# Performance work log

Hardware: AMD Instinct MI355X
Metric: run time of the kernel (lower is better)

Reference implementation:

```python
import jax, jax.numpy as jnp
import numpy as np

B, N, FIN, FOUT, E = 2, 50000, 128, 64, 800000


def setup_inputs() -> dict:
    key = jax.random.key(0)
    ks = jax.random.split(key, 7)
    x = jax.random.normal(ks[0], (B, N, FIN), dtype=jnp.float32)
    W = jax.random.normal(ks[1], (FIN, FOUT), dtype=jnp.float32) * (1.0 / np.sqrt(FIN))
    W_self = jax.random.normal(ks[2], (FIN, FOUT), dtype=jnp.float32) * (1.0 / np.sqrt(FIN))
    b_self = jax.random.normal(ks[3], (FOUT,), dtype=jnp.float32) * 0.01
    edge_row = jax.random.randint(ks[4], (E,), 0, N, dtype=jnp.int32)
    edge_col = jax.random.randint(ks[5], (E,), 0, N, dtype=jnp.int32)
    edge_val = jax.random.uniform(ks[6], (E,), dtype=jnp.float32)
    return {"x": x, "W": W, "W_self": W_self, "b_self": b_self,
            "edge_row": edge_row, "edge_col": edge_col, "edge_val": edge_val}


def reference(x, W, W_self, b_self, edge_row, edge_col, edge_val):
    # x: (B, N, FIN); adjacency in COO form: out[r] += val * in[c]
    Bn, Nn, _ = x.shape
    Fo = W.shape[1]
    x_trans = jnp.einsum("bnf,fo->bno", x, W)               # (B, N, FOUT), no bias
    # Same layout trick as torch: sparse.mm over (N, B*FOUT)
    xr = x_trans.transpose(1, 0, 2).reshape(Nn, Bn * Fo)    # (N, B*FOUT)
    msgs = edge_val[:, None] * xr[edge_col]                  # (E, B*FOUT) gather
    agg = jax.ops.segment_sum(msgs, edge_row, num_segments=Nn)  # (N, B*FOUT) scatter-add
    agg = agg.reshape(Nn, Bn, Fo).transpose(1, 0, 2)         # (B, N, FOUT)
    self_c = jnp.einsum("bnf,fo->bno", x, W_self) + b_self   # Linear with bias
    return jax.nn.relu(self_c + agg)
```

## Files before the change

### kernel.cpp

```cpp
#include <hip/hip_runtime.h>
#include <hip/hip_fp16.h>

#define Bc   2
#define Nn   50000
#define FINc 128
#define FOUTc 64
#define Mtot (Bc * Nn)
#define CCOMB 128
#define GB 1563
#define CAP 64

#define NRNG   128
#define NBUCK  391
#define ABLK   256
#define ATHR   1024
#define RECCAP 3200

typedef __bf16 bf16x8 __attribute__((ext_vector_type(8)));
typedef float  f32x4  __attribute__((ext_vector_type(4)));

static __device__ inline unsigned short f2bf(float f) {
    unsigned int u = __float_as_uint(f);
    u += 0x7fffu + ((u >> 16) & 1u);
    return (unsigned short)(u >> 16);
}

__global__ __launch_bounds__(256) void prep(
    const float* __restrict__ W, const float* __restrict__ Ws,
    unsigned short* __restrict__ Bp)
{
    const int idx = blockIdx.x * 256 + threadIdx.x;
    const int lane = idx & 63;
    const int kt   = (idx >> 6) & 3;
    const int nt   = idx >> 8;
    const int n    = nt * 16 + (lane & 15);
    const int k0   = kt * 32 + (lane >> 4) * 8;
    unsigned short o8[8];
#pragma unroll
    for (int j = 0; j < 8; ++j) {
        const int f = k0 + j;
        const float v = (n < 64) ? W[f * FOUTc + n] : Ws[f * FOUTc + (n - 64)];
        o8[j] = f2bf(v);
    }
    *(uint4*)&Bp[(size_t)idx * 8] = *(uint4*)o8;
}

__global__ __launch_bounds__(256) void gemm(
    const float* __restrict__ x, const unsigned short* __restrict__ Bp,
    const float* __restrict__ bself,
    unsigned short* __restrict__ xrb, float* __restrict__ outp)
{
    const int gb   = blockIdx.x;
    const int lane = threadIdx.x & 63;
    const int quad = lane >> 4;
    const int mbase = gb * 64 + (threadIdx.x >> 6) * 16;

    const int mrow   = mbase + (lane & 15);
    const int mclamp = (mrow < Mtot) ? mrow : (Mtot - 1);
    const float* __restrict__ xrow = &x[(size_t)mclamp * FINc + quad * 8];

    float4 xv[8];
#pragma unroll
    for (int kt = 0; kt < 4; ++kt) {
        xv[2 * kt]     = *(const float4*)&xrow[kt * 32];
        xv[2 * kt + 1] = *(const float4*)&xrow[kt * 32 + 4];
    }

    f32x4 acc[8] = {};

#pragma unroll
    for (int kt = 0; kt < 4; ++kt) {
        const float4 xa = xv[2 * kt];
        const float4 xb = xv[2 * kt + 1];
        bf16x8 bf;
        bf[0] = (__bf16)xa.x; bf[1] = (__bf16)xa.y;
        bf[2] = (__bf16)xa.z; bf[3] = (__bf16)xa.w;
        bf[4] = (__bf16)xb.x; bf[5] = (__bf16)xb.y;
        bf[6] = (__bf16)xb.z; bf[7] = (__bf16)xb.w;

        const bf16x8* __restrict__ abase =
            (const bf16x8*)&Bp[(size_t)(kt * 64 + lane) * 8];
#pragma unroll
        for (int nt = 0; nt < 8; ++nt) {
            const bf16x8 af = abase[nt * 4 * 64];
            acc[nt] = __builtin_amdgcn_mfma_f32_16x16x32_bf16(af, bf, acc[nt], 0, 0, 0);
        }
    }

    const int m = mbase + (lane & 15);
    if (m < Mtot) {
        const int bb = (m >= Nn) ? 1 : 0;
        const int n = m - bb * Nn;
        unsigned short* __restrict__ xp = &xrb[(size_t)n * CCOMB + bb * FOUTc];
        const int cq = quad * 4;
#pragma unroll
        for (int nt = 0; nt < 4; ++nt) {
            const int c = nt * 16 + cq;
            unsigned short h[4];
            h[0] = f2bf(acc[nt][0]); h[1] = f2bf(acc[nt][1]);
            h[2] = f2bf(acc[nt][2]); h[3] = f2bf(acc[nt][3]);
            *(uint2*)&xp[c] = *(uint2*)h;
        }
        float* __restrict__ op = &outp[(size_t)m * FOUTc];
#pragma unroll
        for (int nt = 4; nt < 8; ++nt) {
            const int o = (nt - 4) * 16 + cq;
            const float4 b4 = *(const float4*)&bself[o];
            float4 v;
            v.x = acc[nt][0] + b4.x; v.y = acc[nt][1] + b4.y;
            v.z = acc[nt][2] + b4.z; v.w = acc[nt][3] + b4.w;
            *(float4*)&op[o] = v;
        }
    }
}

__global__ __launch_bounds__(1024) void bin_a(
    const int* __restrict__ erow, const int* __restrict__ ecol,
    const float* __restrict__ evalv, unsigned int* __restrict__ cntm,
    unsigned int* __restrict__ ofsm, uint2* __restrict__ stage,
    int E, int ec)
{
    __shared__ unsigned int hist[512];
    __shared__ unsigned int incl[512];
    __shared__ unsigned int cur[NBUCK];
    __shared__ unsigned int recs[RECCAP * 2];

    const int tid = threadIdx.x;
    const int ord = blockIdx.x;
    const int e0 = ord * ec;
    int e1 = e0 + ec; if (e1 > E) e1 = E;
    if (e1 - e0 > RECCAP) e1 = e0 + RECCAP;
    const int tot = e1 - e0;

    if (tid < 512) hist[tid] = 0u;
    __syncthreads();

    for (int e = e0 + tid; e < e1; e += ATHR)
        atomicAdd(&hist[erow[e] >> 7], 1u);
    __syncthreads();

    if (tid < 512) incl[tid] = hist[tid];
    __syncthreads();
    for (int off = 1; off < 512; off <<= 1) {
        const unsigned int a0 = (tid < 512 && tid >= off) ? incl[tid - off] : 0u;
        __syncthreads();
        if (tid < 512) incl[tid] += a0;
        __syncthreads();
    }

    for (int i = tid; i < NBUCK; i += ATHR) {
        const unsigned int c = hist[i];
        const unsigned int x0 = incl[i] - c;
        cur[i] = x0;
        cntm[(size_t)ord * NBUCK + i] = c;
        ofsm[(size_t)ord * NBUCK + i] = x0;
    }
    __syncthreads();

    for (int e = e0 + tid; e < e1; e += ATHR) {
        const int   r = erow[e];
        const int   c = ecol[e];
        const float v = evalv[e];
        const int  nb = r >> 7;
        const unsigned int k = atomicAdd(&cur[nb], 1u);
        recs[2 * k]     = ((unsigned int)__half_as_ushort(__float2half(v)) << 17) |
                          (unsigned int)c;
        recs[2 * k + 1] = (unsigned int)(r & 127);
    }
    __syncthreads();

    uint2* __restrict__ chunk = &stage[(size_t)ord * RECCAP];
    for (int j = tid; j < tot; j += ATHR)
        chunk[j] = make_uint2(recs[2 * j], recs[2 * j + 1]);
}

__global__ __launch_bounds__(256) void bin_b(
    const unsigned int* __restrict__ cntm, const unsigned int* __restrict__ ofsm,
    const uint2* __restrict__ stage,
    unsigned int* __restrict__ cvp, int* __restrict__ cntp)
{
    __shared__ unsigned int lists[NRNG * CAP];
    __shared__ unsigned int lcnt[NRNG];

    const int tid = threadIdx.x;
    const int nb  = blockIdx.x;
    const int row0 = nb << 7;
    int nrows = Nn - row0; if (nrows > NRNG) nrows = NRNG;

    for (int i = tid; i < NRNG; i += 256) lcnt[i] = 0u;
    __syncthreads();

    {
        const unsigned int c = cntm[(size_t)tid * NBUCK + nb];
        const unsigned int o = ofsm[(size_t)tid * NBUCK + nb];
        const uint2* __restrict__ run = &stage[(size_t)tid * RECCAP + o];
        for (unsigned int j = 0; j < c; ++j) {
            const uint2 rec = run[j];
            const int rl = (int)(rec.y & 127u);
            const unsigned int k = atomicAdd(&lcnt[rl], 1u);
            if (k < CAP) lists[(rl << 6) + k] = rec.x;
        }
    }
    __syncthreads();

    unsigned int* __restrict__ dst = &cvp[(size_t)row0 << 6];
    const int words = nrows << 6;
    for (int i = tid; i < words; i += 256) dst[i] = lists[i];
    for (int rl = tid; rl < nrows; rl += 256) {
        const unsigned int c = lcnt[rl];
        cntp[(size_t)(row0 + rl) * 16] = (int)(c < CAP ? c : CAP);
    }
}

#define GATHP(W, PRED, ACC)                                                   \
    {                                                                         \
        const unsigned int w = (W);                                           \
        unsigned int col = w & 0x1FFFFu;                                      \
        col = (col < Nn) ? col : 0u;           \
        const float vv = (PRED) ? __half2float(__ushort_as_half(              \
                             (unsigned short)(w >> 17))) : 0.0f;              \
        const uint4 raw = *(const uint4*)&xrb[(size_t)col * CCOMB + c0];      \
        ACC[0] = fmaf(vv, __uint_as_float(raw.x << 16),         ACC[0]);      \
        ACC[1] = fmaf(vv, __uint_as_float(raw.x & 0xffff0000u), ACC[1]);      \
        ACC[2] = fmaf(vv, __uint_as_float(raw.y << 16),         ACC[2]);      \
        ACC[3] = fmaf(vv, __uint_as_float(raw.y & 0xffff0000u), ACC[3]);      \
        ACC[4] = fmaf(vv, __uint_as_float(raw.z << 16),         ACC[4]);      \
        ACC[5] = fmaf(vv, __uint_as_float(raw.z & 0xffff0000u), ACC[5]);      \
        ACC[6] = fmaf(vv, __uint_as_float(raw.w << 16),         ACC[6]);      \
        ACC[7] = fmaf(vv, __uint_as_float(raw.w & 0xffff0000u), ACC[7]);      \
    }

__global__ __launch_bounds__(256) void row_gather(
    const int* __restrict__ cntp, const unsigned int* __restrict__ cvp,
    const unsigned short* __restrict__ xrb, float* __restrict__ outp)
{
    const int j    = blockIdx.x;
    const int low3 = j & 7;
    const int h    = (low3 >= 4) ? 1 : 0;
    const int ord  = (j >> 3) * 4 + (low3 & 3);
    int n = ord * 4 + (threadIdx.x >> 6);
    n = __builtin_amdgcn_readfirstlane(n);

    const int lane = threadIdx.x & 63;
    const int slot = lane >> 3;
    const int c0   = h * 64 + (lane & 7) * 8;
    const unsigned int* __restrict__ seg = &cvp[(size_t)n << 6];

    const int kc = min(cntp[(size_t)n * 16], CAP);
    const unsigned int u0 = seg[slot];
    const unsigned int u1 = seg[8 + slot];

    float aA[8] = {0.f, 0.f, 0.f, 0.f, 0.f, 0.f, 0.f, 0.f};

    GATHP(u0, slot < kc,     aA);
    GATHP(u1, slot + 8 < kc, aA);

    for (int e = 16 + slot; e < kc; e += 8) {
        const unsigned int u = seg[e];
        GATHP(u, true, aA);
    }

#pragma unroll
    for (int i = 0; i < 8; ++i) {
        aA[i] += __shfl_down(aA[i], 8);
        aA[i] += __shfl_down(aA[i], 16);
        aA[i] += __shfl_down(aA[i], 32);
    }

    if (lane < 8) {
        const size_t m = (size_t)h * Nn + n;
        const int o = lane * 8;
        float* __restrict__ op = &outp[m * FOUTc + o];
        float4 s0 = *(float4*)&op[0];
        float4 s1 = *(float4*)&op[4];
        s0.x = fmaxf(s0.x + aA[0], 0.0f); s0.y = fmaxf(s0.y + aA[1], 0.0f);
        s0.z = fmaxf(s0.z + aA[2], 0.0f); s0.w = fmaxf(s0.w + aA[3], 0.0f);
        s1.x = fmaxf(s1.x + aA[4], 0.0f); s1.y = fmaxf(s1.y + aA[5], 0.0f);
        s1.z = fmaxf(s1.z + aA[6], 0.0f); s1.w = fmaxf(s1.w + aA[7], 0.0f);
        *(float4*)&op[0] = s0;
        *(float4*)&op[4] = s1;
    }
}

extern "C" void kernel_launch(void* const* d_in, const int* in_sizes, int n_in,
                              void* d_out, int out_size, void* d_ws, size_t ws_size,
                              hipStream_t stream)
{
    const float* x    = (const float*)d_in[0];
    const float* W    = (const float*)d_in[1];
    const float* Ws   = (const float*)d_in[2];
    const float* bs   = (const float*)d_in[3];
    const int*   erow = (const int*)d_in[4];
    const int*   ecol = (const int*)d_in[5];
    const float* eval = (const float*)d_in[6];
    float* outp = (float*)d_out;
    const int E = in_sizes[4];

    unsigned short* xrb = (unsigned short*)d_ws;
    unsigned int*   cvp = (unsigned int*)(xrb + (size_t)Nn * CCOMB);
    int*            cntp = (int*)(cvp + ((size_t)Nn << 6));
    unsigned short* Bp  = (unsigned short*)(cntp + (size_t)Nn * 16);
    unsigned int*   cntm = (unsigned int*)(Bp + 16384);
    unsigned int*   ofsm = cntm + (size_t)ABLK * NBUCK;
    uint2*          stage = (uint2*)(ofsm + (size_t)ABLK * NBUCK);

    const int ec = (E + ABLK - 1) / ABLK;

    prep<<<8, 256, 0, stream>>>(W, Ws, Bp);

    gemm<<<GB, 256, 0, stream>>>(x, Bp, bs, xrb, outp);

    bin_a<<<ABLK, ATHR, 0, stream>>>(erow, ecol, eval, cntm, ofsm, stage, E, ec);

    bin_b<<<NBUCK, 256, 0, stream>>>(cntm, ofsm, stage, cvp, cntp);

    row_gather<<<Nn / 2, 256, 0, stream>>>(cntp, cvp, xrb, outp);
}
```

Before: 178.5 us.

## Fuse per-bucket binning with row gather and shrink buckets to 50 rows

```diff
diff --git a/kernel.cpp b/kernel.cpp
--- a/kernel.cpp
+++ b/kernel.cpp
@@ -10,8 +10,8 @@
 #define GB 1563
 #define CAP 64
 
-#define NRNG   128
-#define NBUCK  391
+#define NRNG   50
+#define NBUCK  1000
 #define ABLK   256
 #define ATHR   1024
 #define RECCAP 3200
@@ -120,8 +120,8 @@
     unsigned int* __restrict__ ofsm, uint2* __restrict__ stage,
     int E, int ec)
 {
-    __shared__ unsigned int hist[512];
-    __shared__ unsigned int incl[512];
+    __shared__ unsigned int hist[1024];
+    __shared__ unsigned int incl[1024];
     __shared__ unsigned int cur[NBUCK];
     __shared__ unsigned int recs[RECCAP * 2];
 
@@ -132,28 +132,28 @@
     if (e1 - e0 > RECCAP) e1 = e0 + RECCAP;
     const int tot = e1 - e0;
 
-    if (tid < 512) hist[tid] = 0u;
+    hist[tid] = 0u;
     __syncthreads();
 
     for (int e = e0 + tid; e < e1; e += ATHR)
-        atomicAdd(&hist[erow[e] >> 7], 1u);
-    __syncthreads();
-
-    if (tid < 512) incl[tid] = hist[tid];
-    __syncthreads();
-    for (int off = 1; off < 512; off <<= 1) {
-        const unsigned int a0 = (tid < 512 && tid >= off) ? incl[tid - off] : 0u;
+        atomicAdd(&hist[erow[e] / NRNG], 1u);
+    __syncthreads();
+
+    incl[tid] = hist[tid];
+    __syncthreads();
+    for (int off = 1; off < 1024; off <<= 1) {
+        const unsigned int a0 = (tid >= off) ? incl[tid - off] : 0u;
         __syncthreads();
-        if (tid < 512) incl[tid] += a0;
+        incl[tid] += a0;
         __syncthreads();
     }
 
-    for (int i = tid; i < NBUCK; i += ATHR) {
-        const unsigned int c = hist[i];
-        const unsigned int x0 = incl[i] - c;
-        cur[i] = x0;
-        cntm[(size_t)ord * NBUCK + i] = c;
-        ofsm[(size_t)ord * NBUCK + i] = x0;
+    if (tid < NBUCK) {
+        const unsigned int c = hist[tid];
+        const unsigned int x0 = incl[tid] - c;
+        cur[tid] = x0;
+        cntm[(size_t)ord * NBUCK + tid] = c;
+        ofsm[(size_t)ord * NBUCK + tid] = x0;
     }
     __syncthreads();
 
@@ -161,55 +161,17 @@
         const int   r = erow[e];
         const int   c = ecol[e];
         const float v = evalv[e];
-        const int  nb = r >> 7;
+        const int  nb = r / NRNG;
         const unsigned int k = atomicAdd(&cur[nb], 1u);
         recs[2 * k]     = ((unsigned int)__half_as_ushort(__float2half(v)) << 17) |
                           (unsigned int)c;
-        recs[2 * k + 1] = (unsigned int)(r & 127);
+        recs[2 * k + 1] = (unsigned int)(r - nb * NRNG);
     }
     __syncthreads();
 
     uint2* __restrict__ chunk = &stage[(size_t)ord * RECCAP];
     for (int j = tid; j < tot; j += ATHR)
         chunk[j] = make_uint2(recs[2 * j], recs[2 * j + 1]);
-}
-
-__global__ __launch_bounds__(256) void bin_b(
-    const unsigned int* __restrict__ cntm, const unsigned int* __restrict__ ofsm,
-    const uint2* __restrict__ stage,
-    unsigned int* __restrict__ cvp, int* __restrict__ cntp)
-{
-    __shared__ unsigned int lists[NRNG * CAP];
-    __shared__ unsigned int lcnt[NRNG];
-
-    const int tid = threadIdx.x;
-    const int nb  = blockIdx.x;
-    const int row0 = nb << 7;
-    int nrows = Nn - row0; if (nrows > NRNG) nrows = NRNG;
-
-    for (int i = tid; i < NRNG; i += 256) lcnt[i] = 0u;
-    __syncthreads();
-
-    {
-        const unsigned int c = cntm[(size_t)tid * NBUCK + nb];
-        const unsigned int o = ofsm[(size_t)tid * NBUCK + nb];
-        const uint2* __restrict__ run = &stage[(size_t)tid * RECCAP + o];
-        for (unsigned int j = 0; j < c; ++j) {
-            const uint2 rec = run[j];
-            const int rl = (int)(rec.y & 127u);
-            const unsigned int k = atomicAdd(&lcnt[rl], 1u);
-            if (k < CAP) lists[(rl << 6) + k] = rec.x;
-        }
-    }
-    __syncthreads();
-
-    unsigned int* __restrict__ dst = &cvp[(size_t)row0 << 6];
-    const int words = nrows << 6;
-    for (int i = tid; i < words; i += 256) dst[i] = lists[i];
-    for (int rl = tid; rl < nrows; rl += 256) {
-        const unsigned int c = lcnt[rl];
-        cntp[(size_t)(row0 + rl) * 16] = (int)(c < CAP ? c : CAP);
-    }
 }
 
 #define GATHP(W, PRED, ACC)                                                   \
@@ -230,55 +192,78 @@
         ACC[7] = fmaf(vv, __uint_as_float(raw.w & 0xffff0000u), ACC[7]);      \
     }
 
-__global__ __launch_bounds__(256) void row_gather(
-    const int* __restrict__ cntp, const unsigned int* __restrict__ cvp,
-    const unsigned short* __restrict__ xrb, float* __restrict__ outp)
-{
-    const int j    = blockIdx.x;
-    const int low3 = j & 7;
-    const int h    = (low3 >= 4) ? 1 : 0;
-    const int ord  = (j >> 3) * 4 + (low3 & 3);
-    int n = ord * 4 + (threadIdx.x >> 6);
-    n = __builtin_amdgcn_readfirstlane(n);
-
-    const int lane = threadIdx.x & 63;
+__global__ __launch_bounds__(1024) void bin_gather(
+    const unsigned int* __restrict__ cntm, const unsigned int* __restrict__ ofsm,
+    const uint2* __restrict__ stage, const unsigned short* __restrict__ xrb,
+    float* __restrict__ outp)
+{
+    __shared__ unsigned int lists[NRNG * CAP];
+    __shared__ unsigned int lcnt[NRNG];
+
+    const int tid = threadIdx.x;
+    const int nb  = blockIdx.x;
+    const int row0 = nb * NRNG;
+
+    if (tid < NRNG) lcnt[tid] = 0u;
+    __syncthreads();
+
+    if (tid < ABLK) {
+        const unsigned int c = cntm[(size_t)tid * NBUCK + nb];
+        const unsigned int o = ofsm[(size_t)tid * NBUCK + nb];
+        const uint2* __restrict__ run = &stage[(size_t)tid * RECCAP + o];
+        for (unsigned int j = 0; j < c; ++j) {
+            const uint2 rec = run[j];
+            const int rl = (int)rec.y;
+            const unsigned int k = atomicAdd(&lcnt[rl], 1u);
+            if (k < CAP) lists[(rl << 6) + k] = rec.x;
+        }
+    }
+    __syncthreads();
+
+    const int wid  = tid >> 6;
+    const int lane = tid & 63;
     const int slot = lane >> 3;
-    const int c0   = h * 64 + (lane & 7) * 8;
-    const unsigned int* __restrict__ seg = &cvp[(size_t)n << 6];
-
-    const int kc = min(cntp[(size_t)n * 16], CAP);
-    const unsigned int u0 = seg[slot];
-    const unsigned int u1 = seg[8 + slot];
-
-    float aA[8] = {0.f, 0.f, 0.f, 0.f, 0.f, 0.f, 0.f, 0.f};
-
-    GATHP(u0, slot < kc,     aA);
-    GATHP(u1, slot + 8 < kc, aA);
-
-    for (int e = 16 + slot; e < kc; e += 8) {
-        const unsigned int u = seg[e];
-        GATHP(u, true, aA);
-    }
-
-#pragma unroll
-    for (int i = 0; i < 8; ++i) {
-        aA[i] += __shfl_down(aA[i], 8);
-        aA[i] += __shfl_down(aA[i], 16);
-        aA[i] += __shfl_down(aA[i], 32);
-    }
-
-    if (lane < 8) {
-        const size_t m = (size_t)h * Nn + n;
-        const int o = lane * 8;
-        float* __restrict__ op = &outp[m * FOUTc + o];
-        float4 s0 = *(float4*)&op[0];
-        float4 s1 = *(float4*)&op[4];
-        s0.x = fmaxf(s0.x + aA[0], 0.0f); s0.y = fmaxf(s0.y + aA[1], 0.0f);
-        s0.z = fmaxf(s0.z + aA[2], 0.0f); s0.w = fmaxf(s0.w + aA[3], 0.0f);
-        s1.x = fmaxf(s1.x + aA[4], 0.0f); s1.y = fmaxf(s1.y + aA[5], 0.0f);
-        s1.z = fmaxf(s1.z + aA[6], 0.0f); s1.w = fmaxf(s1.w + aA[7], 0.0f);
-        *(float4*)&op[0] = s0;
-        *(float4*)&op[4] = s1;
+
+    for (int task = wid; task < NRNG * 2; task += 16) {
+        const int rl = task >> 1;
+        const int h  = task & 1;
+        const int c0 = h * 64 + (lane & 7) * 8;
+        const int rbase = rl << 6;
+
+        const int kc = min((int)lcnt[rl], CAP);
+        const unsigned int u0 = lists[rbase + slot];
+        const unsigned int u1 = lists[rbase + 8 + slot];
+
+        float aA[8] = {0.f, 0.f, 0.f, 0.f, 0.f, 0.f, 0.f, 0.f};
+
+        GATHP(u0, slot < kc,     aA);
+        GATHP(u1, slot + 8 < kc, aA);
+
+        for (int e = 16 + slot; e < kc; e += 8) {
+            const unsigned int u = lists[rbase + e];
+            GATHP(u, true, aA);
+        }
+
+#pragma unroll
+        for (int i = 0; i < 8; ++i) {
+            aA[i] += __shfl_down(aA[i], 8);
+            aA[i] += __shfl_down(aA[i], 16);
+            aA[i] += __shfl_down(aA[i], 32);
+        }
+
+        if (lane < 8) {
+            const size_t m = (size_t)h * Nn + (row0 + rl);
+            const int o = lane * 8;
+            float* __restrict__ op = &outp[m * FOUTc + o];
+            float4 s0 = *(float4*)&op[0];
+            float4 s1 = *(float4*)&op[4];
+            s0.x = fmaxf(s0.x + aA[0], 0.0f); s0.y = fmaxf(s0.y + aA[1], 0.0f);
+            s0.z = fmaxf(s0.z + aA[2], 0.0f); s0.w = fmaxf(s0.w + aA[3], 0.0f);
+            s1.x = fmaxf(s1.x + aA[4], 0.0f); s1.y = fmaxf(s1.y + aA[5], 0.0f);
+            s1.z = fmaxf(s1.z + aA[6], 0.0f); s1.w = fmaxf(s1.w + aA[7], 0.0f);
+            *(float4*)&op[0] = s0;
+            *(float4*)&op[4] = s1;
+        }
     }
 }
 
@@ -297,9 +282,7 @@
     const int E = in_sizes[4];
 
     unsigned short* xrb = (unsigned short*)d_ws;
-    unsigned int*   cvp = (unsigned int*)(xrb + (size_t)Nn * CCOMB);
-    int*            cntp = (int*)(cvp + ((size_t)Nn << 6));
-    unsigned short* Bp  = (unsigned short*)(cntp + (size_t)Nn * 16);
+    unsigned short* Bp  = xrb + (size_t)Nn * CCOMB;
     unsigned int*   cntm = (unsigned int*)(Bp + 16384);
     unsigned int*   ofsm = cntm + (size_t)ABLK * NBUCK;
     uint2*          stage = (uint2*)(ofsm + (size_t)ABLK * NBUCK);
@@ -312,7 +295,5 @@
 
     bin_a<<<ABLK, ATHR, 0, stream>>>(erow, ecol, eval, cntm, ofsm, stage, E, ec);
 
-    bin_b<<<NBUCK, 256, 0, stream>>>(cntm, ofsm, stage, cvp, cntp);
-
-    row_gather<<<Nn / 2, 256, 0, stream>>>(cntp, cvp, xrb, outp);
-}
+    bin_gather<<<NBUCK, ATHR, 0, stream>>>(cntm, ofsm, stage, xrb, outp);
+}
```

Result: no change. 179.4 us (+0.5%).
